# Performance work log

Hardware: AMD Instinct MI355X
Metric: run time of the kernel (lower is better)

## Reference

```python
import jax, jax.numpy as jnp
import numpy as np

B, S, D = 1, 2048, 1024
H, DH = 16, 64
FF_INNER = 4 * D          # 4096
FUSED = 2 * FF_INNER      # 8192
ROT_BASE = 1000.0


def _rope_tables(seq_len, dim_head):
    # rotarizer: inv_freq = (base ** (arange(0, dh, 2)/dh)) ** -1 ; cached in bfloat16
    inv_freq = 1.0 / (ROT_BASE ** (jnp.arange(0, dim_head, 2, dtype=jnp.float32) / dim_head))
    t = jnp.arange(seq_len, dtype=jnp.float32)
    freqs = jnp.outer(t, inv_freq)                     # [S, DH/2]
    cos = jnp.cos(freqs).astype(jnp.bfloat16)[None, :, None, :]  # [1,S,1,DH/2]
    sin = jnp.sin(freqs).astype(jnp.bfloat16)[None, :, None, :]
    return cos, sin


def _apply_rope(x, cos, sin):
    d = x.shape[-1] // 2
    x1, x2 = x[..., :d], x[..., d:]
    y1 = x1 * cos + x2 * sin
    y2 = -x1 * sin + x2 * cos
    return jnp.concatenate([y1, y2], axis=-1).astype(x.dtype)


def _l2norm(x):
    # F.normalize(p=2, dim=-1), eps=1e-12
    n = jnp.linalg.norm(x, axis=-1, keepdims=True)
    return x / jnp.maximum(n, 1e-12)


def setup_inputs() -> dict:
    key = jax.random.key(0)
    ks = jax.random.split(key, 12)
    std = 0.02
    inp = {
        "h_states": jax.random.normal(ks[0], (B, S, D), jnp.float32),
        "Wq": jax.random.normal(ks[1], (D, D), jnp.float32) * std,
        "Wk": jax.random.normal(ks[2], (D, D), jnp.float32) * std,
        "Wv": jax.random.normal(ks[3], (D, D), jnp.float32) * std,
        "Wqb": jax.random.normal(ks[4], (D, D), jnp.float32) * std,
        "Wkb": jax.random.normal(ks[5], (D, D), jnp.float32) * std,
        "Wo": jax.random.normal(ks[6], (D, D), jnp.float32) * std,
        "bo": jnp.zeros((D,), jnp.float32),
        "W1": jax.random.normal(ks[7], (D, FUSED), jnp.float32) * std,
        "b1": jnp.zeros((FUSED,), jnp.float32),
        "W2": jax.random.normal(ks[8], (FF_INNER, D), jnp.float32) * std,
        "b2": jnp.zeros((D,), jnp.float32),
        "learnedlambda": jnp.asarray(1.0, jnp.float32),
        # l2normscale init: log(S^2 - S) for training_seqlen S
        "l2normscale": jnp.asarray(np.log(float(S) ** 2 - float(S)), np.float32),
    }
    return inp


def reference(h_states, Wq, Wk, Wv, Wqb, Wkb, Wo, bo, W1, b1, W2, b2, learnedlambda, l2normscale):
    b, s, d = h_states.shape
    scale = DH ** -0.5

    # layerwisenorm: RMSNorm, no affine
    eps = jnp.finfo(h_states.dtype).eps
    x = h_states * jax.lax.rsqrt(jnp.mean(jnp.square(h_states), axis=-1, keepdims=True) + eps)

    # projections -> [B,S,H,DH]
    def proj(W):
        return (x @ W).reshape(b, s, H, DH)
    q, k, v = proj(Wq), proj(Wk), proj(Wv)
    qb, kb = proj(Wqb), proj(Wkb)

    cos, sin = _rope_tables(s, DH)
    # per-head qk-norm (l2norm) then rope; v untouched
    q = _apply_rope(_l2norm(q), cos, sin)
    k = _apply_rope(_l2norm(k), cos, sin)
    qb = _apply_rope(_l2norm(qb), cos, sin)
    kb = _apply_rope(_l2norm(kb), cos, sin)

    causal = jnp.tril(jnp.ones((s, s), bool))  # [S,S]

    # main attention: scale=1 (l2norm path), causal softmax, scaled by l2normscale
    scores = jnp.einsum("bqhd,bkhd->bhqk", q, k)
    scores = jnp.where(causal[None, None], scores, -jnp.inf)
    attn = jax.nn.softmax(scores, axis=-1)
    y = l2normscale * jnp.einsum("bhqk,bkhd->bhqd", attn, v)  # [B,H,S,DH]

    # bias attention: masked raw scores @ ones == causal row-sum, broadcast over DH
    sb = jnp.einsum("bqhd,bkhd->bhqk", qb, kb) * scale
    sb = jnp.where(causal[None, None], sb, 0.0)
    y = y + jnp.sum(sb, axis=-1, keepdims=True)  # broadcast over head dim

    y = y.transpose(0, 2, 1, 3).reshape(b, s, d)
    attn_out = y @ Wo + bo

    # fused SwiGLU: chunk -> (x_part, gate); silu(gate) * x_part
    u = x @ W1 + b1
    xp, gate = u[..., :FF_INNER], u[..., FF_INNER:]
    ff = (jax.nn.silu(gate) * xp) @ W2 + b2

    return h_states * learnedlambda + ff + attn_out
```

## Files before the change

### kernel.cpp

```cpp
#include <hip/hip_runtime.h>
#include <hip/hip_bf16.h>
#include <math.h>

typedef __bf16 bf16x8 __attribute__((ext_vector_type(8)));
typedef float  f32x4  __attribute__((ext_vector_type(4)));

#define GLD16(g, l) __builtin_amdgcn_global_load_lds(                      \
    (const __attribute__((address_space(1))) void*)(g),                    \
    (__attribute__((address_space(3))) void*)(l), 16, 0, 0)


__device__ __forceinline__ void tconv_tile(const float* __restrict__ in,
                                           __bf16* __restrict__ out,
                                           int ldin, int ldout,
                                           int r0, int c0, int tid) {
  __shared__ float t[32][33];
  int tx = tid & 31, ty = tid >> 5;
  #pragma unroll
  for (int i = ty; i < 32; i += 8)
    t[i][tx] = in[(size_t)(r0 + i) * ldin + c0 + tx];
  __syncthreads();
  #pragma unroll
  for (int i = ty; i < 32; i += 8)
    out[(size_t)(c0 + i) * ldout + r0 + tx] = (__bf16)t[tx][i];
}

__global__ __launch_bounds__(256) void tconv_k(const float* __restrict__ in,
                                               __bf16* __restrict__ out,
                                               int ldin, int ldout) {
  tconv_tile(in, out, ldin, ldout, blockIdx.y * 32, blockIdx.x * 32, threadIdx.x);
}

__global__ __launch_bounds__(256) void tconvw1p_k(const float* __restrict__ W1,
                                                  __bf16* __restrict__ out) {
  int c0 = blockIdx.x * 32;
  int src_c0 = ((c0 >> 5) & 1) * 4096 + (c0 >> 6) * 32;
  __shared__ float t[32][33];
  int r0 = blockIdx.y * 32;
  int tid = threadIdx.x, tx = tid & 31, ty = tid >> 5;
  #pragma unroll
  for (int i = ty; i < 32; i += 8)
    t[i][tx] = W1[(size_t)(r0 + i) * 8192 + src_c0 + tx];
  __syncthreads();
  #pragma unroll
  for (int i = ty; i < 32; i += 8)
    out[(size_t)(c0 + i) * 1024 + r0 + tx] = (__bf16)t[tx][i];
}

__global__ __launch_bounds__(256) void tconv5_k(const float* __restrict__ w0,
    const float* __restrict__ w1, const float* __restrict__ w2,
    const float* __restrict__ w3, const float* __restrict__ w4,
    __bf16* __restrict__ out) {
  const float* src[5] = {w0, w1, w2, w3, w4};
  int z = blockIdx.z;
  tconv_tile(src[z], out + (size_t)z * 1048576, 1024, 1024,
             blockIdx.y * 32, blockIdx.x * 32, threadIdx.x);
}

__global__ __launch_bounds__(256) void tconvwow2_k(const float* __restrict__ Wo,
    const float* __restrict__ W2, __bf16* __restrict__ WoW2t) {
  int tid = threadIdx.x;
  if (blockIdx.z == 0) {
    if (blockIdx.y >= 32) return;
    __shared__ float t[32][33];
    int r0 = blockIdx.y * 32, c0 = blockIdx.x * 32;
    int tx = tid & 31, ty = tid >> 5;
    #pragma unroll
    for (int i = ty; i < 32; i += 8)
      t[i][tx] = Wo[(size_t)(r0 + i) * 1024 + c0 + tx];
    __syncthreads();
    #pragma unroll
    for (int i = ty; i < 32; i += 8)
      WoW2t[(size_t)(c0 + i) * 5120 + r0 + tx] = (__bf16)t[tx][i];
  } else {
    __shared__ float t[32][33];
    int r0 = blockIdx.y * 32, c0 = blockIdx.x * 32;
    int tx = tid & 31, ty = tid >> 5;
    #pragma unroll
    for (int i = ty; i < 32; i += 8)
      t[i][tx] = W2[(size_t)(r0 + i) * 1024 + c0 + tx];
    __syncthreads();
    #pragma unroll
    for (int i = ty; i < 32; i += 8)
      WoW2t[(size_t)(c0 + i) * 5120 + 1024 + r0 + tx] = (__bf16)t[tx][i];
  }
}

__global__ __launch_bounds__(256) void rmsnorm_k(const float* __restrict__ hs,
                                                 __bf16* __restrict__ x) {
  int row = blockIdx.x, tid = threadIdx.x;
  const float4 v = ((const float4*)(hs + (size_t)row * 1024))[tid];
  float ss = v.x * v.x + v.y * v.y + v.z * v.z + v.w * v.w;
  #pragma unroll
  for (int o = 32; o > 0; o >>= 1) ss += __shfl_xor(ss, o);
  __shared__ float ps[4];
  if ((tid & 63) == 0) ps[tid >> 6] = ss;
  __syncthreads();
  float tot = ps[0] + ps[1] + ps[2] + ps[3];
  float r = rsqrtf(tot * (1.0f / 1024.0f) + 1.1920929e-7f);
  __bf16* xr = x + (size_t)row * 1024 + tid * 4;
  xr[0] = (__bf16)(v.x * r); xr[1] = (__bf16)(v.y * r);
  xr[2] = (__bf16)(v.z * r); xr[3] = (__bf16)(v.w * r);
}

__global__ __launch_bounds__(256) void gemm_bt_k(
    const __bf16* __restrict__ A, const __bf16* __restrict__ Bt,
    float* __restrict__ C, int N, int K) {
  __shared__ __bf16 sA[2][128 * 32];
  __shared__ __bf16 sB[2][128 * 32];
  const int tid = threadIdx.x;
  const int lane = tid & 63;
  const int quad = lane >> 4, l16 = lane & 15;
  const int wave = tid >> 6;
  const int waveM = wave >> 1, waveN = wave & 1;
  const int m0 = blockIdx.y * 128, n0 = blockIdx.x * 128;
  const int nk = K >> 5;
  const int rowS = tid >> 2;
  const int kg = ((tid & 3) ^ ((rowS >> 1) & 3)) * 8;
  const __bf16* gA0 = A + (size_t)(m0 + rowS) * K + kg;
  const __bf16* gA1 = gA0 + (size_t)64 * K;
  const __bf16* gB0 = Bt + (size_t)(n0 + rowS) * K + kg;
  const __bf16* gB1 = gB0 + (size_t)64 * K;
  const int lo0 = tid * 8, lo1 = 2048 + tid * 8;

  GLD16(gA0, sA[0] + lo0);
  GLD16(gA1, sA[0] + lo1);
  GLD16(gB0, sB[0] + lo0);
  GLD16(gB1, sB[0] + lo1);

  f32x4 acc[4][4] = {};
  for (int i = 0; i < nk; ++i) {
    __syncthreads();
    if (i + 1 < nk) {
      const int k = (i + 1) * 32;
      __bf16* dA = sA[(i + 1) & 1];
      __bf16* dB = sB[(i + 1) & 1];
      GLD16(gA0 + k, dA + lo0);
      GLD16(gA1 + k, dA + lo1);
      GLD16(gB0 + k, dB + lo0);
      GLD16(gB1 + k, dB + lo1);
    }
    const __bf16* cA = sA[i & 1];
    const __bf16* cB = sB[i & 1];
    bf16x8 af[4], bfv[4];
    #pragma unroll
    for (int mt = 0; mt < 4; ++mt) {
      int r = waveM * 64 + mt * 16 + l16;
      af[mt] = *(const bf16x8*)(cA + r * 32 + ((quad ^ ((r >> 1) & 3)) * 8));
    }
    #pragma unroll
    for (int nt = 0; nt < 4; ++nt) {
      int r = waveN * 64 + nt * 16 + l16;
      bfv[nt] = *(const bf16x8*)(cB + r * 32 + ((quad ^ ((r >> 1) & 3)) * 8));
    }
    #pragma unroll
    for (int mt = 0; mt < 4; ++mt)
      #pragma unroll
      for (int nt = 0; nt < 4; ++nt)
        acc[mt][nt] = __builtin_amdgcn_mfma_f32_16x16x32_bf16(af[mt], bfv[nt], acc[mt][nt], 0, 0, 0);
  }
  #pragma unroll
  for (int mt = 0; mt < 4; ++mt) {
    int row = m0 + waveM * 64 + mt * 16 + quad * 4;
    #pragma unroll
    for (int nt = 0; nt < 4; ++nt) {
      int col = n0 + waveN * 64 + nt * 16 + l16;
      #pragma unroll
      for (int r = 0; r < 4; ++r)
        C[(size_t)(row + r) * N + col] = acc[mt][nt][r];
    }
  }
}

__global__ __launch_bounds__(256) void gemm_partk_k(
    const __bf16* __restrict__ A, const __bf16* __restrict__ Bt,
    float* __restrict__ P, int N, int K) {
  __shared__ __bf16 sA[2][128 * 32];
  __shared__ __bf16 sB[2][128 * 32];
  const int tid = threadIdx.x;
  const int lane = tid & 63;
  const int quad = lane >> 4, l16 = lane & 15;
  const int wave = tid >> 6;
  const int waveM = wave >> 1, waveN = wave & 1;
  const int m0 = blockIdx.y * 128, n0 = blockIdx.x * 128;
  const int kz = blockIdx.z, nz = gridDim.z;
  const int kper = K / nz, kbeg = kz * kper;
  const int nk = kper >> 5;
  const size_t MN = (size_t)gridDim.y * 128 * N;
  float* C = P + (size_t)kz * MN;
  const int rowS = tid >> 2;
  const int kg = ((tid & 3) ^ ((rowS >> 1) & 3)) * 8;
  const __bf16* gA0 = A + (size_t)(m0 + rowS) * K + kbeg + kg;
  const __bf16* gA1 = gA0 + (size_t)64 * K;
  const __bf16* gB0 = Bt + (size_t)(n0 + rowS) * K + kbeg + kg;
  const __bf16* gB1 = gB0 + (size_t)64 * K;
  const int lo0 = tid * 8, lo1 = 2048 + tid * 8;

  GLD16(gA0, sA[0] + lo0);
  GLD16(gA1, sA[0] + lo1);
  GLD16(gB0, sB[0] + lo0);
  GLD16(gB1, sB[0] + lo1);

  f32x4 acc[4][4] = {};
  for (int i = 0; i < nk; ++i) {
    __syncthreads();
    if (i + 1 < nk) {
      const int k = (i + 1) * 32;
      __bf16* dA = sA[(i + 1) & 1];
      __bf16* dB = sB[(i + 1) & 1];
      GLD16(gA0 + k, dA + lo0);
      GLD16(gA1 + k, dA + lo1);
      GLD16(gB0 + k, dB + lo0);
      GLD16(gB1 + k, dB + lo1);
    }
    const __bf16* cA = sA[i & 1];
    const __bf16* cB = sB[i & 1];
    bf16x8 af[4], bfv[4];
    #pragma unroll
    for (int mt = 0; mt < 4; ++mt) {
      int r = waveM * 64 + mt * 16 + l16;
      af[mt] = *(const bf16x8*)(cA + r * 32 + ((quad ^ ((r >> 1) & 3)) * 8));
    }
    #pragma unroll
    for (int nt = 0; nt < 4; ++nt) {
      int r = waveN * 64 + nt * 16 + l16;
      bfv[nt] = *(const bf16x8*)(cB + r * 32 + ((quad ^ ((r >> 1) & 3)) * 8));
    }
    #pragma unroll
    for (int mt = 0; mt < 4; ++mt)
      #pragma unroll
      for (int nt = 0; nt < 4; ++nt)
        acc[mt][nt] = __builtin_amdgcn_mfma_f32_16x16x32_bf16(af[mt], bfv[nt], acc[mt][nt], 0, 0, 0);
  }
  #pragma unroll
  for (int mt = 0; mt < 4; ++mt) {
    int row = m0 + waveM * 64 + mt * 16 + quad * 4;
    #pragma unroll
    for (int nt = 0; nt < 4; ++nt) {
      int col = n0 + waveN * 64 + nt * 16 + l16;
      #pragma unroll
      for (int r = 0; r < 4; ++r)
        C[(size_t)(row + r) * N + col] = acc[mt][nt][r];
    }
  }
}

__global__ __launch_bounds__(512, 2) void ffn1silu_k(
    const __bf16* __restrict__ A, const __bf16* __restrict__ W1t,
    const float* __restrict__ b1, __bf16* __restrict__ ffout) {
  __shared__ __bf16 sA[4][256 * 32];
  __shared__ __bf16 sB[4][256 * 32];
  const int tid = threadIdx.x, lane = tid & 63, w = tid >> 6;
  const int quad = lane >> 4, l16 = lane & 15;
  const int wm = w >> 2, wn = w & 3;
  const int m0 = blockIdx.y * 256;
  const int n0p = blockIdx.x * 256;
  const int K = 1024, NKT = 32;
  const int rowS = tid >> 2;
  const int kg = ((tid & 3) ^ ((rowS >> 1) & 3)) * 8;
  const __bf16* gA0 = A + (size_t)(m0 + rowS) * K + kg;
  const __bf16* gA1 = gA0 + (size_t)128 * K;
  const __bf16* gB0 = W1t + (size_t)(n0p + rowS) * K + kg;
  const __bf16* gB1 = gB0 + (size_t)128 * K;
  const int lo0 = tid * 8, lo1 = 4096 + tid * 8;

  f32x4 acc[8][4] = {};

  auto stageA = [&](int t) {
    __bf16* d = sA[t & 3];
    GLD16(gA0 + t * 32, d + lo0);
    GLD16(gA1 + t * 32, d + lo1);
  };
  auto stageB = [&](int t) {
    __bf16* d = sB[t & 3];
    GLD16(gB0 + t * 32, d + lo0);
    GLD16(gB1 + t * 32, d + lo1);
  };

  auto compute_half = [&](const __bf16* cA, const __bf16* cB,
                          const bf16x8* bfr, int half) {
    bf16x8 af[4];
    #pragma unroll
    for (int mt = 0; mt < 4; ++mt) {
      int r = wm * 128 + half * 64 + mt * 16 + l16;
      af[mt] = *(const bf16x8*)(cA + r * 32 + ((quad ^ ((r >> 1) & 3)) * 8));
    }
    __builtin_amdgcn_s_setprio(1);
    #pragma unroll
    for (int mt = 0; mt < 4; ++mt)
      #pragma unroll
      for (int nt = 0; nt < 4; ++nt)
        acc[half * 4 + mt][nt] = __builtin_amdgcn_mfma_f32_16x16x32_bf16(
            af[mt], bfr[nt], acc[half * 4 + mt][nt], 0, 0, 0);
    __builtin_amdgcn_s_setprio(0);
  };

  stageA(0); stageB(0);
  stageA(1); stageB(1);
  stageA(2); stageB(2);

  #pragma unroll 1
  for (int t = 0; t < NKT; ++t) {
    if (t < NKT - 2)
      asm volatile("s_waitcnt vmcnt(8)" ::: "memory");
    else if (t == NKT - 2)
      asm volatile("s_waitcnt vmcnt(4)" ::: "memory");
    else
      asm volatile("s_waitcnt vmcnt(0)" ::: "memory");
    __builtin_amdgcn_s_barrier();
    __builtin_amdgcn_sched_barrier(0);
    const __bf16* cA = sA[t & 3];
    const __bf16* cB = sB[t & 3];
    if (t + 3 < NKT) stageA(t + 3);
    bf16x8 bfr[4];
    #pragma unroll
    for (int nt = 0; nt < 4; ++nt) {
      int r = wn * 64 + nt * 16 + l16;
      bfr[nt] = *(const bf16x8*)(cB + r * 32 + ((quad ^ ((r >> 1) & 3)) * 8));
    }
    compute_half(cA, cB, bfr, 0);
    if (t + 3 < NKT) stageB(t + 3);
    compute_half(cA, cB, bfr, 1);
  }

  const int colbase = (blockIdx.x * 4 + wn) * 32;
  #pragma unroll
  for (int j = 0; j < 8; ++j) {
    int row = m0 + wm * 128 + (j >> 2) * 64 + (j & 3) * 16 + quad * 4;
    #pragma unroll
    for (int p = 0; p < 2; ++p) {
      int col = colbase + p * 16 + l16;
      float bxv = b1[col], bgv = b1[col + 4096];
      #pragma unroll
      for (int r = 0; r < 4; ++r) {
        float xp = acc[j][p][r] + bxv;
        float g  = acc[j][p + 2][r] + bgv;
        float val = xp * g / (1.f + __expf(-g));
        ffout[(size_t)(row + r) * 5120 + 1024 + col] = (__bf16)val;
      }
    }
  }
}

__global__ __launch_bounds__(256) void combine_k(
    const float* __restrict__ P, const float* __restrict__ b2,
    const float* __restrict__ bo, const float* __restrict__ hs,
    const float* __restrict__ plam, float* __restrict__ out) {
  const size_t MN = (size_t)2048 * 1024;
  size_t i = ((size_t)blockIdx.x * 256 + threadIdx.x) * 4;
  int col = (int)(i & 1023);
  float4 a0 = *(const float4*)(P + i);
  float4 a1 = *(const float4*)(P + MN + i);
  float4 a2 = *(const float4*)(P + 2 * MN + i);
  float4 a3 = *(const float4*)(P + 3 * MN + i);
  float4 h  = *(const float4*)(hs + i);
  float4 v2 = *(const float4*)(b2 + col);
  float4 vo = *(const float4*)(bo + col);
  float lam = plam[0];
  float4 o;
  o.x = (a0.x + a1.x) + (a2.x + a3.x) + v2.x + vo.x + lam * h.x;
  o.y = (a0.y + a1.y) + (a2.y + a3.y) + v2.y + vo.y + lam * h.y;
  o.z = (a0.z + a1.z) + (a2.z + a3.z) + v2.z + vo.z + lam * h.z;
  o.w = (a0.w + a1.w) + (a2.w + a3.w) + v2.w + vo.w + lam * h.w;
  *(float4*)(out + i) = o;
}

__global__ __launch_bounds__(256) void qkprep_k(const float* __restrict__ proj,
    __bf16* __restrict__ qo, __bf16* __restrict__ ko,
    float* __restrict__ qbo, float* __restrict__ kbo) {
  int gw = blockIdx.x * 4 + (threadIdx.x >> 6);
  int lane = threadIdx.x & 63;
  int s = gw >> 4, h = gw & 15;
  int j = lane & 31;
  float inv = powf(1000.0f, -(float)j * (1.0f / 32.0f));
  float ang = (float)s * inv;
  float cb = (float)(__bf16)cosf(ang);
  float sb = (float)(__bf16)sinf(ang);
  size_t ibase = (size_t)s * 5120 + h * 64 + lane;
  size_t obase = (size_t)s * 1024 + h * 64 + lane;
  bool lo = lane < 32;

  auto proc = [&](const float* src) -> float {
    float xv = src[ibase];
    float ss = xv * xv;
    #pragma unroll
    for (int o = 32; o > 0; o >>= 1) ss += __shfl_xor(ss, o);
    float y = xv / fmaxf(sqrtf(ss), 1e-12f);
    float yp = __shfl_xor(y, 32);
    return lo ? (y * cb + yp * sb) : (y * cb - yp * sb);
  };
  qo[obase]  = (__bf16)proc(proj + 0);
  ko[obase]  = (__bf16)proc(proj + 1024);
  qbo[obase] = proc(proj + 3072);
  kbo[obase] = proc(proj + 4096);
}

__global__ __launch_bounds__(64) void kbsum_k(const float* __restrict__ kb,
                                              float* __restrict__ tsum) {
  int t = blockIdx.x, h = blockIdx.y, d = threadIdx.x;
  size_t base = (size_t)h * 64 + d;
  float s = 0.f;
  #pragma unroll 4
  for (int r = 0; r < 32; ++r)
    s += kb[(size_t)(t * 32 + r) * 1024 + base];
  tsum[(t * 16 + h) * 64 + d] = s;
}

__global__ __launch_bounds__(64) void sbrow2_k(const float* __restrict__ qb,
                                               const float* __restrict__ kb,
                                               const float* __restrict__ tsum,
                                               float* __restrict__ sb) {
  int t = blockIdx.x, h = blockIdx.y, d = threadIdx.x;
  size_t base = (size_t)h * 64 + d;
  float run = 0.f;
  for (int tp = 0; tp < t; ++tp) run += tsum[(tp * 16 + h) * 64 + d];
  for (int s0 = 0; s0 < 32; s0 += 4) {
    float p[4];
    #pragma unroll
    for (int u = 0; u < 4; ++u) {
      size_t off = (size_t)(t * 32 + s0 + u) * 1024 + base;
      run += kb[off];
      p[u] = qb[off] * run;
    }
    #pragma unroll
    for (int o = 32; o > 0; o >>= 1) {
      #pragma unroll
      for (int u = 0; u < 4; ++u) p[u] += __shfl_xor(p[u], o);
    }
    if (d == 0) {
      #pragma unroll
      for (int u = 0; u < 4; ++u) sb[(t * 32 + s0 + u) * 16 + h] = 0.125f * p[u];
    }
  }
}

__global__ __launch_bounds__(256) void attn_k(const __bf16* __restrict__ qg,
    const __bf16* __restrict__ kg, const __bf16* __restrict__ vtg,
    float* __restrict__ o_part, float* __restrict__ m_part,
    float* __restrict__ l_part) {
  __shared__ __bf16 sK[64 * 64];
  __shared__ __bf16 sVt[64 * 64];
  __shared__ __bf16 sP[4][16 * 64];
  const int pair = blockIdx.x, j4 = blockIdx.y, hh = blockIdx.z;
  const int tid = threadIdx.x, lane = tid & 63, w = tid >> 6;
  const int quad = lane >> 4, l16 = lane & 15;
  const int srow = tid >> 3;
  const int sg = (tid & 7) ^ (srow & 7);
  __bf16* ldsK = sK + tid * 8;
  __bf16* ldsV = sVt + tid * 8;
  __bf16* sPw = sP[w];

  for (int phase = 0; phase < 2; ++phase) {
    const int qt = phase ? 31 - pair : pair;
    const int q0 = qt * 64;
    const int n = qt + 1;
    const int kb = (j4 * n) >> 2, ke = ((j4 + 1) * n) >> 2;
    bf16x8 qf[2];
    #pragma unroll
    for (int kk = 0; kk < 2; ++kk)
      qf[kk] = *(const bf16x8*)(qg + (size_t)(q0 + w * 16 + l16) * 1024 + hh * 64 + kk * 32 + quad * 8);
    f32x4 accO[4] = {};
    float m_[4], l_[4];
    #pragma unroll
    for (int r = 0; r < 4; ++r) { m_[r] = -INFINITY; l_[r] = 0.f; }

    for (int kt = kb; kt < ke; ++kt) {
      const __bf16* gK = kg + (size_t)(kt * 64 + srow) * 1024 + hh * 64 + sg * 8;
      const __bf16* gV = vtg + (size_t)(hh * 64 + srow) * 2048 + kt * 64 + sg * 8;
      GLD16(gK, ldsK);
      GLD16(gK + (size_t)32 * 1024, ldsK + 2048);
      GLD16(gV, ldsV);
      GLD16(gV + (size_t)32 * 2048, ldsV + 2048);
      __syncthreads();

      f32x4 s4[4];
      #pragma unroll
      for (int nt = 0; nt < 4; ++nt) {
        int r = nt * 16 + l16;
        bf16x8 b0 = *(const bf16x8*)(sK + r * 64 + ((quad ^ (r & 7)) * 8));
        bf16x8 b1 = *(const bf16x8*)(sK + r * 64 + (((4 + quad) ^ (r & 7)) * 8));
        f32x4 sa = {0.f, 0.f, 0.f, 0.f};
        sa = __builtin_amdgcn_mfma_f32_16x16x32_bf16(qf[0], b0, sa, 0, 0, 0);
        sa = __builtin_amdgcn_mfma_f32_16x16x32_bf16(qf[1], b1, sa, 0, 0, 0);
        s4[nt] = sa;
      }
      if (kt == qt) {
        #pragma unroll
        for (int nt = 0; nt < 4; ++nt)
          #pragma unroll
          for (int r = 0; r < 4; ++r)
            if (nt * 16 + l16 > w * 16 + quad * 4 + r) s4[nt][r] = -INFINITY;
      }
      float mx[4], al[4], rs[4];
      #pragma unroll
      for (int r = 0; r < 4; ++r)
        mx[r] = fmaxf(fmaxf(s4[0][r], s4[1][r]), fmaxf(s4[2][r], s4[3][r]));
      #pragma unroll
      for (int o = 1; o < 16; o <<= 1)
        #pragma unroll
        for (int r = 0; r < 4; ++r) mx[r] = fmaxf(mx[r], __shfl_xor(mx[r], o));
      #pragma unroll
      for (int r = 0; r < 4; ++r) {
        float mn = fmaxf(m_[r], mx[r]);
        al[r] = __expf(m_[r] - mn);
        m_[r] = mn;
      }
      float p[4][4];
      #pragma unroll
      for (int nt = 0; nt < 4; ++nt)
        #pragma unroll
        for (int r = 0; r < 4; ++r)
          p[nt][r] = __expf(s4[nt][r] - m_[r]);
      #pragma unroll
      for (int r = 0; r < 4; ++r)
        rs[r] = (p[0][r] + p[1][r]) + (p[2][r] + p[3][r]);
      #pragma unroll
      for (int o = 1; o < 16; o <<= 1)
        #pragma unroll
        for (int r = 0; r < 4; ++r) rs[r] += __shfl_xor(rs[r], o);
      #pragma unroll
      for (int r = 0; r < 4; ++r) l_[r] = l_[r] * al[r] + rs[r];
      #pragma unroll
      for (int nt = 0; nt < 4; ++nt)
        #pragma unroll
        for (int r = 0; r < 4; ++r) accO[nt][r] *= al[r];
      #pragma unroll
      for (int nt = 0; nt < 4; ++nt)
        #pragma unroll
        for (int r = 0; r < 4; ++r) {
          int row = quad * 4 + r, col = nt * 16 + l16;
          sPw[row * 64 + (col ^ ((row & 7) << 3))] = (__bf16)p[nt][r];
        }
      #pragma unroll
      for (int kk = 0; kk < 2; ++kk) {
        bf16x8 a = *(const bf16x8*)(sPw + l16 * 64 + (((kk * 4 + quad) ^ (l16 & 7)) * 8));
        #pragma unroll
        for (int nt = 0; nt < 4; ++nt) {
          int vr = nt * 16 + l16;
          bf16x8 bv = *(const bf16x8*)(sVt + vr * 64 + (((kk * 4 + quad) ^ (vr & 7)) * 8));
          accO[nt] = __builtin_amdgcn_mfma_f32_16x16x32_bf16(a, bv, accO[nt], 0, 0, 0);
        }
      }
      __syncthreads();
    }
    #pragma unroll
    for (int r = 0; r < 4; ++r) {
      int grow = q0 + w * 16 + quad * 4 + r;
      if (l16 == 0) {
        m_part[((size_t)j4 * 2048 + grow) * 16 + hh] = m_[r];
        l_part[((size_t)j4 * 2048 + grow) * 16 + hh] = l_[r];
      }
      #pragma unroll
      for (int nt = 0; nt < 4; ++nt)
        o_part[((size_t)j4 * 2048 + grow) * 1024 + hh * 64 + nt * 16 + l16] = accO[nt][r];
    }
  }
}

__global__ __launch_bounds__(256) void attnmerge_k(const float* __restrict__ o_part,
    const float* __restrict__ m_part, const float* __restrict__ l_part,
    const float* __restrict__ sbr, const float* __restrict__ pl2s,
    __bf16* __restrict__ yo) {
  int idx = blockIdx.x * 256 + threadIdx.x;
  int s = idx >> 8, rem = idx & 255;
  int h = rem >> 4, dg = (rem & 15) * 4;
  float m[4], l[4];
  #pragma unroll
  for (int j = 0; j < 4; ++j) {
    m[j] = m_part[((size_t)j * 2048 + s) * 16 + h];
    l[j] = l_part[((size_t)j * 2048 + s) * 16 + h];
  }
  float M = fmaxf(fmaxf(m[0], m[1]), fmaxf(m[2], m[3]));
  float den = 0.f;
  float4 acc = {0.f, 0.f, 0.f, 0.f};
  #pragma unroll
  for (int j = 0; j < 4; ++j) {
    float e = __expf(m[j] - M);
    den += l[j] * e;
    float4 o = *(const float4*)(o_part + ((size_t)j * 2048 + s) * 1024 + h * 64 + dg);
    acc.x += e * o.x; acc.y += e * o.y; acc.z += e * o.z; acc.w += e * o.w;
  }
  float sc = pl2s[0] / den;
  float add = sbr[s * 16 + h];
  __bf16* yp = yo + (size_t)s * 5120 + h * 64 + dg;
  yp[0] = (__bf16)(sc * acc.x + add);
  yp[1] = (__bf16)(sc * acc.y + add);
  yp[2] = (__bf16)(sc * acc.z + add);
  yp[3] = (__bf16)(sc * acc.w + add);
}

extern "C" void kernel_launch(void* const* d_in, const int* in_sizes, int n_in,
                              void* d_out, int out_size, void* d_ws, size_t ws_size,
                              hipStream_t stream) {
  (void)in_sizes; (void)n_in; (void)out_size; (void)ws_size;
  const float* hs   = (const float*)d_in[0];
  const float* Wq   = (const float*)d_in[1];
  const float* Wk   = (const float*)d_in[2];
  const float* Wv   = (const float*)d_in[3];
  const float* Wqb  = (const float*)d_in[4];
  const float* Wkb  = (const float*)d_in[5];
  const float* Wo   = (const float*)d_in[6];
  const float* bo   = (const float*)d_in[7];
  const float* W1   = (const float*)d_in[8];
  const float* b1   = (const float*)d_in[9];
  const float* W2   = (const float*)d_in[10];
  const float* b2   = (const float*)d_in[11];
  const float* plam = (const float*)d_in[12];
  const float* pl2s = (const float*)d_in[13];
  float* out = (float*)d_out;
  char* ws = (char*)d_ws;

  size_t off = 0;
  auto alloc = [&](size_t bytes) { char* p = ws + off; off += (bytes + 255) & ~(size_t)255; return p; };
  __bf16* Wt5    = (__bf16*)alloc((size_t)5 * 1024 * 1024 * 2);
  __bf16* WoW2t  = (__bf16*)alloc((size_t)1024 * 5120 * 2);
  __bf16* W1t    = (__bf16*)alloc((size_t)8192 * 1024 * 2);
  __bf16* xbf    = (__bf16*)alloc((size_t)2048 * 1024 * 2);
  __bf16* concat = (__bf16*)alloc((size_t)2048 * 5120 * 2);
  float*  proj  = (float*)alloc((size_t)2048 * 5120 * 4);
  float*  qbf32 = (float*)alloc((size_t)2048 * 1024 * 4);
  float*  kbf32 = (float*)alloc((size_t)2048 * 1024 * 4);
  __bf16* qbf   = (__bf16*)alloc((size_t)2048 * 1024 * 2);
  __bf16* kbf   = (__bf16*)alloc((size_t)2048 * 1024 * 2);
  float*  o_part = proj;
  float*  m_part = qbf32;
  float*  l_part = qbf32 + (size_t)4 * 2048 * 16;
  float*  gpart  = proj;
  __bf16* vtbf  = (__bf16*)alloc((size_t)1024 * 2048 * 2);
  float*  sbrow = (float*)alloc((size_t)2048 * 16 * 4);
  float*  tsum  = (float*)alloc((size_t)64 * 16 * 64 * 4);

  tconv5_k<<<dim3(32, 32, 5), 256, 0, stream>>>(Wq, Wk, Wv, Wqb, Wkb, Wt5);
  tconvwow2_k<<<dim3(32, 128, 2), 256, 0, stream>>>(Wo, W2, WoW2t);
  tconvw1p_k<<<dim3(256, 32), 256, 0, stream>>>(W1, W1t);

  rmsnorm_k<<<2048, 256, 0, stream>>>(hs, xbf);
  gemm_bt_k<<<dim3(40, 16), 256, 0, stream>>>(xbf, Wt5, proj, 5120, 1024);
  qkprep_k<<<8192, 256, 0, stream>>>(proj, qbf, kbf, qbf32, kbf32);
  tconv_k<<<dim3(32, 64), 256, 0, stream>>>(proj + 2048, vtbf, 5120, 2048);
  kbsum_k<<<dim3(64, 16), 64, 0, stream>>>(kbf32, tsum);
  sbrow2_k<<<dim3(64, 16), 64, 0, stream>>>(qbf32, kbf32, tsum, sbrow);
  attn_k<<<dim3(16, 4, 16), 256, 0, stream>>>(qbf, kbf, vtbf, o_part, m_part, l_part);
  attnmerge_k<<<2048, 256, 0, stream>>>(o_part, m_part, l_part, sbrow, pl2s, concat);
  ffn1silu_k<<<dim3(32, 8), 512, 0, stream>>>(xbf, W1t, b1, concat);
  gemm_partk_k<<<dim3(8, 16, 4), 256, 0, stream>>>(concat, WoW2t, gpart, 1024, 5120);
  combine_k<<<2048, 256, 0, stream>>>(gpart, b2, bo, hs, plam, out);
}
```

Baseline: 368.2 us.

## Deepen GEMM LDS pipeline to four stages with explicit vmcnt waits

Both bf16 GEMM kernels (full-K and split-K) move from a double-buffered shared-memory ring to a four-slot ring with three tiles in flight. Each iteration now waits with explicit s_waitcnt vmcnt counts plus a raw s_barrier instead of __syncthreads. The MFMA block is wrapped in s_setprio to favour math issue. The aim is to hide global-to-LDS load latency behind more compute; in exchange each block uses twice the LDS (64KB), and the manual wait counts assume no other outstanding vector memory ops.

Result: slower. 387.0 us (+5.1%).

```diff
diff --git a/kernel.cpp b/kernel.cpp
--- a/kernel.cpp
+++ b/kernel.cpp
@@ -103,11 +103,11 @@
   xr[2] = (__bf16)(v.z * r); xr[3] = (__bf16)(v.w * r);
 }
 
-__global__ __launch_bounds__(256) void gemm_bt_k(
+__global__ __launch_bounds__(256, 2) void gemm_bt_k(
     const __bf16* __restrict__ A, const __bf16* __restrict__ Bt,
     float* __restrict__ C, int N, int K) {
-  __shared__ __bf16 sA[2][128 * 32];
-  __shared__ __bf16 sB[2][128 * 32];
+  __shared__ __bf16 sA[4][128 * 32];
+  __shared__ __bf16 sB[4][128 * 32];
   const int tid = threadIdx.x;
   const int lane = tid & 63;
   const int quad = lane >> 4, l16 = lane & 15;
@@ -123,25 +123,30 @@
   const __bf16* gB1 = gB0 + (size_t)64 * K;
   const int lo0 = tid * 8, lo1 = 2048 + tid * 8;
 
-  GLD16(gA0, sA[0] + lo0);
-  GLD16(gA1, sA[0] + lo1);
-  GLD16(gB0, sB[0] + lo0);
-  GLD16(gB1, sB[0] + lo1);
+  auto stage = [&](int t) {
+    __bf16* dA = sA[t & 3];
+    __bf16* dB = sB[t & 3];
+    GLD16(gA0 + t * 32, dA + lo0);
+    GLD16(gA1 + t * 32, dA + lo1);
+    GLD16(gB0 + t * 32, dB + lo0);
+    GLD16(gB1 + t * 32, dB + lo1);
+  };
+  stage(0); stage(1); stage(2);
 
   f32x4 acc[4][4] = {};
+  #pragma unroll 1
   for (int i = 0; i < nk; ++i) {
-    __syncthreads();
-    if (i + 1 < nk) {
-      const int k = (i + 1) * 32;
-      __bf16* dA = sA[(i + 1) & 1];
-      __bf16* dB = sB[(i + 1) & 1];
-      GLD16(gA0 + k, dA + lo0);
-      GLD16(gA1 + k, dA + lo1);
-      GLD16(gB0 + k, dB + lo0);
-      GLD16(gB1 + k, dB + lo1);
-    }
-    const __bf16* cA = sA[i & 1];
-    const __bf16* cB = sB[i & 1];
+    if (i < nk - 2)
+      asm volatile("s_waitcnt vmcnt(8)" ::: "memory");
+    else if (i == nk - 2)
+      asm volatile("s_waitcnt vmcnt(4)" ::: "memory");
+    else
+      asm volatile("s_waitcnt vmcnt(0)" ::: "memory");
+    __builtin_amdgcn_s_barrier();
+    __builtin_amdgcn_sched_barrier(0);
+    const __bf16* cA = sA[i & 3];
+    const __bf16* cB = sB[i & 3];
+    if (i + 3 < nk) stage(i + 3);
     bf16x8 af[4], bfv[4];
     #pragma unroll
     for (int mt = 0; mt < 4; ++mt) {
@@ -153,11 +158,13 @@
       int r = waveN * 64 + nt * 16 + l16;
       bfv[nt] = *(const bf16x8*)(cB + r * 32 + ((quad ^ ((r >> 1) & 3)) * 8));
     }
+    __builtin_amdgcn_s_setprio(1);
     #pragma unroll
     for (int mt = 0; mt < 4; ++mt)
       #pragma unroll
       for (int nt = 0; nt < 4; ++nt)
         acc[mt][nt] = __builtin_amdgcn_mfma_f32_16x16x32_bf16(af[mt], bfv[nt], acc[mt][nt], 0, 0, 0);
+    __builtin_amdgcn_s_setprio(0);
   }
   #pragma unroll
   for (int mt = 0; mt < 4; ++mt) {
@@ -172,11 +179,11 @@
   }
 }
 
-__global__ __launch_bounds__(256) void gemm_partk_k(
+__global__ __launch_bounds__(256, 2) void gemm_partk_k(
     const __bf16* __restrict__ A, const __bf16* __restrict__ Bt,
     float* __restrict__ P, int N, int K) {
-  __shared__ __bf16 sA[2][128 * 32];
-  __shared__ __bf16 sB[2][128 * 32];
+  __shared__ __bf16 sA[4][128 * 32];
+  __shared__ __bf16 sB[4][128 * 32];
   const int tid = threadIdx.x;
   const int lane = tid & 63;
   const int quad = lane >> 4, l16 = lane & 15;
@@ -196,25 +203,30 @@
   const __bf16* gB1 = gB0 + (size_t)64 * K;
   const int lo0 = tid * 8, lo1 = 2048 + tid * 8;
 
-  GLD16(gA0, sA[0] + lo0);
-  GLD16(gA1, sA[0] + lo1);
-  GLD16(gB0, sB[0] + lo0);
-  GLD16(gB1, sB[0] + lo1);
+  auto stage = [&](int t) {
+    __bf16* dA = sA[t & 3];
+    __bf16* dB = sB[t & 3];
+    GLD16(gA0 + t * 32, dA + lo0);
+    GLD16(gA1 + t * 32, dA + lo1);
+    GLD16(gB0 + t * 32, dB + lo0);
+    GLD16(gB1 + t * 32, dB + lo1);
+  };
+  stage(0); stage(1); stage(2);
 
   f32x4 acc[4][4] = {};
+  #pragma unroll 1
   for (int i = 0; i < nk; ++i) {
-    __syncthreads();
-    if (i + 1 < nk) {
-      const int k = (i + 1) * 32;
-      __bf16* dA = sA[(i + 1) & 1];
-      __bf16* dB = sB[(i + 1) & 1];
-      GLD16(gA0 + k, dA + lo0);
-      GLD16(gA1 + k, dA + lo1);
-      GLD16(gB0 + k, dB + lo0);
-      GLD16(gB1 + k, dB + lo1);
-    }
-    const __bf16* cA = sA[i & 1];
-    const __bf16* cB = sB[i & 1];
+    if (i < nk - 2)
+      asm volatile("s_waitcnt vmcnt(8)" ::: "memory");
+    else if (i == nk - 2)
+      asm volatile("s_waitcnt vmcnt(4)" ::: "memory");
+    else
+      asm volatile("s_waitcnt vmcnt(0)" ::: "memory");
+    __builtin_amdgcn_s_barrier();
+    __builtin_amdgcn_sched_barrier(0);
+    const __bf16* cA = sA[i & 3];
+    const __bf16* cB = sB[i & 3];
+    if (i + 3 < nk) stage(i + 3);
     bf16x8 af[4], bfv[4];
     #pragma unroll
     for (int mt = 0; mt < 4; ++mt) {
@@ -226,11 +238,13 @@
       int r = waveN * 64 + nt * 16 + l16;
       bfv[nt] = *(const bf16x8*)(cB + r * 32 + ((quad ^ ((r >> 1) & 3)) * 8));
     }
+    __builtin_amdgcn_s_setprio(1);
     #pragma unroll
     for (int mt = 0; mt < 4; ++mt)
       #pragma unroll
       for (int nt = 0; nt < 4; ++nt)
         acc[mt][nt] = __builtin_amdgcn_mfma_f32_16x16x32_bf16(af[mt], bfv[nt], acc[mt][nt], 0, 0, 0);
+    __builtin_amdgcn_s_setprio(0);
   }
   #pragma unroll
   for (int mt = 0; mt < 4; ++mt) {
```
